# Kernel optimization log

Hardware: AMD Instinct MI355X
Metric: run time of the kernel (lower is better)

## Reference

```python
import jax, jax.numpy as jnp
import numpy as np

B, T, C = 2, 2048, 1024
NUM_HEADS, QK_LEN, V_LEN = 16, 64, 64


def setup_inputs() -> dict:
    key = jax.random.key(0)
    ks = jax.random.split(key, 11)
    s = 0.02
    return {
        "Q": jax.random.normal(ks[0], (B, T, C), jnp.float32),
        "K": jax.random.normal(ks[1], (B, T, C), jnp.float32),
        "V": jax.random.normal(ks[2], (B, T, C), jnp.float32),
        # Linear weights stored as (in, out); y = x @ W + b
        "Wq": jax.random.normal(ks[3], (C, NUM_HEADS * QK_LEN), jnp.float32) * s,
        "bq": jnp.zeros((NUM_HEADS * QK_LEN,), jnp.float32),
        "Wk": jax.random.normal(ks[4], (C, NUM_HEADS * QK_LEN), jnp.float32) * s,
        "bk": jnp.zeros((NUM_HEADS * QK_LEN,), jnp.float32),
        "Wv": jax.random.normal(ks[5], (C, NUM_HEADS * V_LEN), jnp.float32) * s,
        "bv": jnp.zeros((NUM_HEADS * V_LEN,), jnp.float32),
        "Wo": jax.random.normal(ks[6], (NUM_HEADS * V_LEN, C), jnp.float32) * s,
        "bo": jnp.zeros((C,), jnp.float32),
    }


def _split_heads(x, n_heads, d):
    b, t, _ = x.shape
    return x.reshape(b, t, n_heads, d).transpose(0, 2, 1, 3)  # (B,H,T,d)


def reference(Q, K, V, Wq, bq, Wk, bk, Wv, bv, Wo, bo):
    q = _split_heads(Q @ Wq + bq, NUM_HEADS, QK_LEN)   # (B,H,T,dk)
    k = _split_heads(K @ Wk + bk, NUM_HEADS, QK_LEN)   # (B,H,T,dk)
    v = _split_heads(V @ Wv + bv, NUM_HEADS, V_LEN)    # (B,H,T,dv)

    scale = 1.0 / jnp.sqrt(jnp.asarray(QK_LEN, q.dtype))
    scores = jnp.einsum("bhqd,bhkd->bhqk", q, k) * scale  # (B,H,T,T)
    attn = jax.nn.softmax(scores, axis=-1)
    out = jnp.einsum("bhqk,bhkd->bhqd", attn, v)           # (B,H,T,dv)

    out = out.transpose(0, 2, 1, 3).reshape(Q.shape[0], Q.shape[1], NUM_HEADS * V_LEN)
    return out @ Wo + bo
```

## Files before the change

### kernel.cpp

```cpp
#include <hip/hip_runtime.h>
#include <hip/hip_bf16.h>
#include <math.h>

constexpr int B = 2, T = 2048, C = 1024, H = 16, D = 64;
constexpr int M = B * T;
constexpr float SCALE_L2E = 0.125f * 1.4426950408889634f;

typedef __attribute__((ext_vector_type(8))) short s16x8;
typedef __attribute__((ext_vector_type(4))) short s16x4;
typedef __attribute__((ext_vector_type(4))) float fv4;

typedef unsigned short ushort_t;

static __device__ __forceinline__ ushort_t f2bf(float x) {
    union { float f; unsigned u; } c; c.f = x;
    unsigned u = c.u + 0x7FFFu + ((c.u >> 16) & 1u);
    return (ushort_t)(u >> 16);
}

static __device__ __forceinline__ int cvt_pk_bf16(float lo, float hi) {
    int r;
    asm("v_cvt_pk_bf16_f32 %0, %1, %2" : "=v"(r) : "v"(lo), "v"(hi));
    return r;
}

#define GLDS(gp, lp) __builtin_amdgcn_global_load_lds( \
    (const __attribute__((address_space(1))) void*)(gp), \
    (__attribute__((address_space(3))) void*)(lp), 16, 0, 0)

__global__ __launch_bounds__(256) void convert_qkv(
    const float* __restrict__ Q, const float* __restrict__ K,
    const float* __restrict__ V, ushort_t* __restrict__ dst)
{
    size_t e = ((size_t)blockIdx.x * 256 + threadIdx.x) * 8;
    const float* src;
    size_t base;
    if (e < (size_t)M * C)          { src = Q; base = 0; }
    else if (e < 2 * (size_t)M * C) { src = K; base = (size_t)M * C; }
    else                            { src = V; base = 2 * (size_t)M * C; }
    const float* p = src + (e - base);
    float4 a = *(const float4*)p;
    float4 b = *(const float4*)(p + 4);
    union { s16x8 v; int i[4]; } o;
    o.i[0] = cvt_pk_bf16(a.x, a.y);
    o.i[1] = cvt_pk_bf16(a.z, a.w);
    o.i[2] = cvt_pk_bf16(b.x, b.y);
    o.i[3] = cvt_pk_bf16(b.z, b.w);
    *(s16x8*)(dst + e) = o.v;
}

__global__ __launch_bounds__(256) void transpose_w(
    const float* __restrict__ W0, const float* __restrict__ W1,
    const float* __restrict__ W2, const float* __restrict__ W3,
    ushort_t* __restrict__ Wt)
{
    const int s = blockIdx.z;
    const float* W = (s == 0) ? W0 : (s == 1) ? W1 : (s == 2) ? W2 : W3;
    const int k0 = blockIdx.x * 64, n0 = blockIdx.y * 64;
    __shared__ ushort_t tile[64][72];
    const int tid = threadIdx.x;
#pragma unroll
    for (int it = 0; it < 4; it++) {
        int f = it * 256 + tid;
        int r = f >> 4, c4 = (f & 15) * 4;
        float4 x = *(const float4*)(W + (size_t)(k0 + r) * C + n0 + c4);
        *(int*)&tile[r][c4]     = cvt_pk_bf16(x.x, x.y);
        *(int*)&tile[r][c4 + 2] = cvt_pk_bf16(x.z, x.w);
    }
    __syncthreads();
#pragma unroll
    for (int it = 0; it < 4; it++) {
        int f = it * 256 + tid;
        int rr = f >> 4, c4 = (f & 15) * 4;
        union { s16x4 v; ushort_t u[4]; } u;
#pragma unroll
        for (int j = 0; j < 4; j++) u.u[j] = tile[c4 + j][rr];
        *(s16x4*)(Wt + (size_t)(s * 1024 + n0 + rr) * 1024 + k0 + c4) = u.v;
    }
}

__global__ __launch_bounds__(256) void transpose_v(
    const ushort_t* __restrict__ vw, ushort_t* __restrict__ vt)
{
    __shared__ ushort_t tile[64][72];
    const int tid = threadIdx.x;
    const int t0 = blockIdx.x * 64;
    const int bh = blockIdx.y;
    const ushort_t* src = vw + ((size_t)bh * T + t0) * D;
#pragma unroll
    for (int it = 0; it < 2; it++) {
        int f = it * 256 + tid;
        int row = f >> 3, c8 = (f & 7) * 8;
        *(s16x8*)&tile[row][c8] = *(const s16x8*)(src + (size_t)row * D + c8);
    }
    __syncthreads();
    ushort_t* dst = vt + (size_t)bh * D * T + t0;
#pragma unroll
    for (int it = 0; it < 4; it++) {
        int f = it * 256 + tid;
        int d = f >> 4, t4 = (f & 15) * 4;
        union { s16x4 v; ushort_t u[4]; } u;
#pragma unroll
        for (int j = 0; j < 4; j++) u.u[j] = tile[t4 + j][d];
        *(s16x4*)(dst + (size_t)d * T + t4) = u.v;
    }
}

__global__ __launch_bounds__(256) void gemm_qkv(
    const ushort_t* __restrict__ qkv, const ushort_t* __restrict__ Wt,
    const float* __restrict__ bq, const float* __restrict__ bk,
    const float* __restrict__ bv,
    ushort_t* __restrict__ qw, ushort_t* __restrict__ kw,
    ushort_t* __restrict__ vw)
{
    __shared__ ushort_t As[2][128 * 32];
    __shared__ ushort_t Bs[2][128 * 32];

    const int tid = threadIdx.x;
    const int w = tid >> 6, lane = tid & 63;
    const int quad = lane >> 4, lc = lane & 15;
    const int wm = w & 1, wn = w >> 1;

    const int nt = blockIdx.x;
    const int m0 = blockIdx.y * 128;
    const int s = nt >> 3;
    const int nsec0 = (nt & 7) * 128;

    const ushort_t* Abase = qkv + (size_t)s * M * C;
    const ushort_t* Btbase = Wt + (size_t)nt * 128 * 1024;

    const int srow = (w << 4) + (lane >> 2);
    const int ske  = (lane & 3) * 8;

    fv4 acc[4][4] = {};

    auto stage = [&](int k0, int buf) {
#pragma unroll
        for (int i = 0; i < 2; i++) {
            int row = i * 64 + srow;
            GLDS(Abase + (size_t)(m0 + row) * 1024 + k0 + ske,
                 As[buf] + i * 2048 + w * 512);
            GLDS(Btbase + (size_t)row * 1024 + k0 + ske,
                 Bs[buf] + i * 2048 + w * 512);
        }
    };

    stage(0, 0);
    __syncthreads();

    for (int k0 = 0; k0 < 1024; k0 += 32) {
        const int cur = (k0 >> 5) & 1;
        if (k0 + 32 < 1024) stage(k0 + 32, cur ^ 1);

        s16x8 af[4], bf[4];
#pragma unroll
        for (int ms = 0; ms < 4; ms++)
            af[ms] = *(const s16x8*)(As[cur] + (wm * 64 + ms * 16 + lc) * 32 + quad * 8);
#pragma unroll
        for (int ns = 0; ns < 4; ns++)
            bf[ns] = *(const s16x8*)(Bs[cur] + (wn * 64 + ns * 16 + lc) * 32 + quad * 8);
#pragma unroll
        for (int ms = 0; ms < 4; ms++)
#pragma unroll
            for (int ns = 0; ns < 4; ns++)
                acc[ms][ns] = __builtin_amdgcn_mfma_f32_16x16x32_bf16(
                    af[ms], bf[ns], acc[ms][ns], 0, 0, 0);
        __syncthreads();
    }

    const float* biasp = (s == 0) ? bq : (s == 1) ? bk : bv;
    const float premul = (s == 0) ? SCALE_L2E : 1.0f;
    ushort_t* outp = (s == 0) ? qw : (s == 1) ? kw : vw;

#pragma unroll
    for (int ns = 0; ns < 4; ns++) {
        const int nl = nsec0 + wn * 64 + ns * 16 + lc;
        const float bias = biasp[nl];
        const int h_ = nl >> 6, d_ = nl & 63;
#pragma unroll
        for (int ms = 0; ms < 4; ms++) {
#pragma unroll
            for (int r = 0; r < 4; r++) {
                int m = m0 + wm * 64 + ms * 16 + quad * 4 + r;
                float val = (acc[ms][ns][r] + bias) * premul;
                int b_ = m >> 11, t_ = m & (T - 1);
                size_t bh = (size_t)(b_ * H + h_);
                outp[((bh * T + t_) << 6) + d_] = f2bf(val);
            }
        }
    }
}

__global__ __launch_bounds__(256) void gemm_final(
    const ushort_t* __restrict__ A, const ushort_t* __restrict__ Wot,
    const float* __restrict__ bo, float* __restrict__ out)
{
    __shared__ ushort_t As[2][128 * 32];
    __shared__ ushort_t Bs[2][64 * 32];

    const int tid = threadIdx.x;
    const int w = tid >> 6, lane = tid & 63;
    const int quad = lane >> 4, lc = lane & 15;
    const int wm = w & 1, wn = w >> 1;

    const int n0 = blockIdx.x * 64;
    const int m0 = blockIdx.y * 128;

    const int srow = (w << 4) + (lane >> 2);
    const int ske  = (lane & 3) * 8;

    fv4 acc[4][2] = {};

    auto stage = [&](int k0, int buf) {
        GLDS(A + (size_t)(m0 + srow) * 1024 + k0 + ske,      As[buf] + w * 512);
        GLDS(A + (size_t)(m0 + 64 + srow) * 1024 + k0 + ske, As[buf] + 2048 + w * 512);
        GLDS(Wot + (size_t)(n0 + srow) * 1024 + k0 + ske,    Bs[buf] + w * 512);
    };

    stage(0, 0);
    __syncthreads();

    for (int k0 = 0; k0 < 1024; k0 += 32) {
        const int cur = (k0 >> 5) & 1;
        if (k0 + 32 < 1024) stage(k0 + 32, cur ^ 1);

        s16x8 af[4], bf[2];
#pragma unroll
        for (int ms = 0; ms < 4; ms++)
            af[ms] = *(const s16x8*)(As[cur] + (wm * 64 + ms * 16 + lc) * 32 + quad * 8);
#pragma unroll
        for (int ns = 0; ns < 2; ns++)
            bf[ns] = *(const s16x8*)(Bs[cur] + (wn * 32 + ns * 16 + lc) * 32 + quad * 8);
#pragma unroll
        for (int ms = 0; ms < 4; ms++)
#pragma unroll
            for (int ns = 0; ns < 2; ns++)
                acc[ms][ns] = __builtin_amdgcn_mfma_f32_16x16x32_bf16(
                    af[ms], bf[ns], acc[ms][ns], 0, 0, 0);
        __syncthreads();
    }

#pragma unroll
    for (int ns = 0; ns < 2; ns++) {
        const int n = n0 + wn * 32 + ns * 16 + lc;
        const float bias = bo[n];
#pragma unroll
        for (int ms = 0; ms < 4; ms++) {
#pragma unroll
            for (int r = 0; r < 4; r++) {
                int m = m0 + wm * 64 + ms * 16 + quad * 4 + r;
                out[(size_t)m * 1024 + n] = acc[ms][ns][r] + bias;
            }
        }
    }
}

__global__ __launch_bounds__(256, 4) void attn(
    const ushort_t* __restrict__ q, const ushort_t* __restrict__ k,
    const ushort_t* __restrict__ vT, ushort_t* __restrict__ o)
{
    __shared__ alignas(16) ushort_t ks[2][64 * 64];
    __shared__ alignas(16) ushort_t vs[2][64 * 64];

    const int tid = threadIdx.x;
    const int w = tid >> 6, lane = tid & 63;
    const int quad = lane >> 4, lc = lane & 15;
    const int cs = lc & 7;
    const int qsub = w & 1, ksub = w >> 1;

    const int id = blockIdx.y * 32 + blockIdx.x;
    const int qt = (id >> 3) & 31;
    const int bh = (id & 7) * 4 + (id >> 8);

    s16x8 aq[2][2];
    const ushort_t* qb = q + ((size_t)bh * T + qt * 64 + qsub * 32) * D;
#pragma unroll
    for (int j = 0; j < 2; j++)
#pragma unroll
        for (int h = 0; h < 2; h++)
            aq[j][h] = *(const s16x8*)(qb + (size_t)(j * 16 + lc) * D + h * 32 + quad * 8);

    fv4 accO[2][4] = {};
    float psum[2] = {0.f, 0.f};

    const ushort_t* kb0 = k + (size_t)bh * T * D;
    const ushort_t* vb0 = vT + (size_t)bh * D * T;

    const int sr8 = lane >> 3;
    const int sch = (lane & 7) ^ sr8;

    auto stage = [&](int kt, int buf) {
#pragma unroll
        for (int i = 0; i < 2; i++) {
            const int r = w * 16 + i * 8 + sr8;
            GLDS(kb0 + (size_t)(kt * 64 + r) * 64 + sch * 8,
                 ks[buf] + (w * 16 + i * 8) * 64);
            GLDS(vb0 + (size_t)r * T + kt * 64 + sch * 8,
                 vs[buf] + (w * 16 + i * 8) * 64);
        }
    };

    stage(0, 0);
    __syncthreads();

    for (int kt = 0; kt < T / 64; kt++) {
        const int cur = kt & 1;
        if (kt + 1 < T / 64) stage(kt + 1, cur ^ 1);

        fv4 accST[2][2] = {};
        __builtin_amdgcn_s_setprio(1);
#pragma unroll
        for (int t4k = 0; t4k < 2; t4k++) {
            const int row = ksub * 32 + t4k * 16 + lc;
            s16x8 ak0 = *(const s16x8*)(ks[cur] + row * 64 + ((quad ^ cs) << 3));
            s16x8 ak1 = *(const s16x8*)(ks[cur] + row * 64 + (((quad + 4) ^ cs) << 3));
#pragma unroll
            for (int j = 0; j < 2; j++) {
                accST[j][t4k] = __builtin_amdgcn_mfma_f32_16x16x32_bf16(
                    ak0, aq[j][0], accST[j][t4k], 0, 0, 0);
                accST[j][t4k] = __builtin_amdgcn_mfma_f32_16x16x32_bf16(
                    ak1, aq[j][1], accST[j][t4k], 0, 0, 0);
            }
        }
        __builtin_amdgcn_s_setprio(0);

        s16x8 av[4];
#pragma unroll
        for (int t4v = 0; t4v < 4; t4v++) {
            const int row = t4v * 16 + lc;
            av[t4v] = *(const s16x8*)(vs[cur] + row * 64 + (((ksub * 4 + quad) ^ cs) << 3));
        }

#pragma unroll
        for (int j = 0; j < 2; j++) {
            float p0 = __builtin_amdgcn_exp2f(accST[j][0][0]);
            float p1 = __builtin_amdgcn_exp2f(accST[j][0][1]);
            float p2 = __builtin_amdgcn_exp2f(accST[j][0][2]);
            float p3 = __builtin_amdgcn_exp2f(accST[j][0][3]);
            float p4 = __builtin_amdgcn_exp2f(accST[j][1][0]);
            float p5 = __builtin_amdgcn_exp2f(accST[j][1][1]);
            float p6 = __builtin_amdgcn_exp2f(accST[j][1][2]);
            float p7 = __builtin_amdgcn_exp2f(accST[j][1][3]);
            psum[j] += ((p0 + p1) + (p2 + p3)) + ((p4 + p5) + (p6 + p7));

            int W00 = cvt_pk_bf16(p0, p1);
            int W01 = cvt_pk_bf16(p2, p3);
            int W10 = cvt_pk_bf16(p4, p5);
            int W11 = cvt_pk_bf16(p6, p7);
            asm("v_permlane32_swap_b32 %0, %1" : "+v"(W00), "+v"(W10));
            asm("v_permlane16_swap_b32 %0, %1" : "+v"(W00), "+v"(W10));
            asm("v_permlane32_swap_b32 %0, %1" : "+v"(W01), "+v"(W11));
            asm("v_permlane16_swap_b32 %0, %1" : "+v"(W01), "+v"(W11));

            union { int i[4]; s16x8 v; } pbu;
            pbu.i[0] = W00; pbu.i[1] = W01; pbu.i[2] = W10; pbu.i[3] = W11;

            __builtin_amdgcn_s_setprio(1);
#pragma unroll
            for (int t4v = 0; t4v < 4; t4v++)
                accO[j][t4v] = __builtin_amdgcn_mfma_f32_16x16x32_bf16(
                    av[t4v], pbu.v, accO[j][t4v], 0, 0, 0);
            __builtin_amdgcn_s_setprio(0);
        }

        __syncthreads();
    }

#pragma unroll
    for (int j = 0; j < 2; j++) {
        psum[j] += __shfl_xor(psum[j], 16);
        psum[j] += __shfl_xor(psum[j], 32);
    }

    float* sc = (float*)&ks[0][0];
#pragma unroll
    for (int c = 0; c < 4; c++) {
        const int j = c >> 1, tv = (c & 1) * 2;
        __syncthreads();
        if (ksub == 1) {
            *(fv4*)(sc + ((qsub * 64 + lane) * 8))     = accO[j][tv];
            *(fv4*)(sc + ((qsub * 64 + lane) * 8 + 4)) = accO[j][tv + 1];
        }
        __syncthreads();
        if (ksub == 0) {
            accO[j][tv]     += *(fv4*)(sc + ((qsub * 64 + lane) * 8));
            accO[j][tv + 1] += *(fv4*)(sc + ((qsub * 64 + lane) * 8 + 4));
        }
    }
    __syncthreads();
    if (ksub == 1) {
        sc[(qsub * 64 + lane) * 2]     = psum[0];
        sc[(qsub * 64 + lane) * 2 + 1] = psum[1];
    }
    __syncthreads();
    if (ksub == 0) {
        psum[0] += sc[(qsub * 64 + lane) * 2];
        psum[1] += sc[(qsub * 64 + lane) * 2 + 1];

        const int b_ = bh >> 4, h_ = bh & 15;
#pragma unroll
        for (int j = 0; j < 2; j++) {
            float inv = 1.0f / psum[j];
            int row = qt * 64 + qsub * 32 + j * 16 + lc;
            ushort_t* op = o + ((size_t)b_ * T + row) * C + h_ * 64;
#pragma unroll
            for (int t4v = 0; t4v < 4; t4v++) {
                union { s16x4 v; int i[2]; } u;
                u.i[0] = cvt_pk_bf16(accO[j][t4v][0] * inv, accO[j][t4v][1] * inv);
                u.i[1] = cvt_pk_bf16(accO[j][t4v][2] * inv, accO[j][t4v][3] * inv);
                *(s16x4*)(op + t4v * 16 + quad * 4) = u.v;
            }
        }
    }
}

extern "C" void kernel_launch(void* const* d_in, const int* in_sizes, int n_in,
                              void* d_out, int out_size, void* d_ws, size_t ws_size,
                              hipStream_t stream)
{
    const float* Q  = (const float*)d_in[0];
    const float* K  = (const float*)d_in[1];
    const float* V  = (const float*)d_in[2];
    const float* Wq = (const float*)d_in[3];
    const float* bq = (const float*)d_in[4];
    const float* Wk = (const float*)d_in[5];
    const float* bk = (const float*)d_in[6];
    const float* Wv = (const float*)d_in[7];
    const float* bv = (const float*)d_in[8];
    const float* Wo = (const float*)d_in[9];
    const float* bo = (const float*)d_in[10];
    float* out = (float*)d_out;

    ushort_t* qkvbf = (ushort_t*)d_ws;
    ushort_t* Wt = qkvbf + (size_t)3 * M * C;
    ushort_t* qw = Wt + (size_t)4096 * 1024;
    ushort_t* kw = qw + (size_t)M * C;
    ushort_t* vw = kw + (size_t)M * C;
    ushort_t* vt = vw + (size_t)M * C;
    ushort_t* ow = qkvbf;
    ushort_t* Wot = Wt + (size_t)3072 * 1024;

    dim3 blk(256);
    convert_qkv<<<dim3(3 * M * C / 2048), blk, 0, stream>>>(Q, K, V, qkvbf);
    transpose_w<<<dim3(16, 16, 4), blk, 0, stream>>>(Wq, Wk, Wv, Wo, Wt);
    gemm_qkv<<<dim3(24, 32), blk, 0, stream>>>(qkvbf, Wt, bq, bk, bv, qw, kw, vw);
    transpose_v<<<dim3(T / 64, B * H), blk, 0, stream>>>(vw, vt);
    attn<<<dim3(T / 64, B * H), blk, 0, stream>>>(qw, kw, vt, ow);
    gemm_final<<<dim3(16, 32), blk, 0, stream>>>(ow, Wot, bo, out);
}
```

Before: 235.7 us.

## Give each wave a private key slice and drop per-tile block barriers

Attention work is redistributed so each of the four waves processes all 64 queries against its own 16-key slice of every 64-key tile. Each wave stages its K and V^T slice into its own LDS region and waits with s_waitcnt on its own loads, so the per-iteration __syncthreads is gone. The catch is that the P·V MFMA is fed half-zero operands, which doubles P·V MFMA issue. Register use also rises (accO[4][4]), so launch bounds drop to 3 blocks, and the end-of-kernel cross-wave reduction of four partial outputs through LDS is larger.

```diff
diff --git a/kernel.cpp b/kernel.cpp
--- a/kernel.cpp
+++ b/kernel.cpp
@@ -255,98 +255,78 @@
     }
 }
 
-__global__ __launch_bounds__(256, 4) void attn(
+__global__ __launch_bounds__(256, 3) void attn(
     const ushort_t* __restrict__ q, const ushort_t* __restrict__ k,
     const ushort_t* __restrict__ vT, ushort_t* __restrict__ o)
 {
-    __shared__ alignas(16) ushort_t ks[2][64 * 64];
-    __shared__ alignas(16) ushort_t vs[2][64 * 64];
+    __shared__ alignas(16) ushort_t ks[2][4][1024];
+    __shared__ alignas(16) ushort_t vs[2][4][1024];
 
     const int tid = threadIdx.x;
     const int w = tid >> 6, lane = tid & 63;
     const int quad = lane >> 4, lc = lane & 15;
     const int cs = lc & 7;
-    const int qsub = w & 1, ksub = w >> 1;
 
     const int id = blockIdx.y * 32 + blockIdx.x;
     const int qt = (id >> 3) & 31;
     const int bh = (id & 7) * 4 + (id >> 8);
 
-    s16x8 aq[2][2];
-    const ushort_t* qb = q + ((size_t)bh * T + qt * 64 + qsub * 32) * D;
-#pragma unroll
-    for (int j = 0; j < 2; j++)
+    s16x8 aq[4][2];
+    const ushort_t* qb = q + ((size_t)bh * T + qt * 64) * D;
+#pragma unroll
+    for (int j = 0; j < 4; j++)
 #pragma unroll
         for (int h = 0; h < 2; h++)
             aq[j][h] = *(const s16x8*)(qb + (size_t)(j * 16 + lc) * D + h * 32 + quad * 8);
 
-    fv4 accO[2][4] = {};
-    float psum[2] = {0.f, 0.f};
-
-    const ushort_t* kb0 = k + (size_t)bh * T * D;
-    const ushort_t* vb0 = vT + (size_t)bh * D * T;
-
-    const int sr8 = lane >> 3;
-    const int sch = (lane & 7) ^ sr8;
+    fv4 accO[4][4] = {};
+    float psum[4] = {0.f, 0.f, 0.f, 0.f};
+
+    const ushort_t* kb0 = k + (size_t)bh * T * D
+        + (size_t)(w * 16 + (lane >> 3)) * 64 + (((lane & 7) ^ ((lane >> 3) & 7)) * 8);
+    const ushort_t* vb0 = vT + (size_t)bh * D * T
+        + (size_t)(lane >> 1) * T + w * 16 + (lane & 1) * 8;
 
     auto stage = [&](int kt, int buf) {
-#pragma unroll
-        for (int i = 0; i < 2; i++) {
-            const int r = w * 16 + i * 8 + sr8;
-            GLDS(kb0 + (size_t)(kt * 64 + r) * 64 + sch * 8,
-                 ks[buf] + (w * 16 + i * 8) * 64);
-            GLDS(vb0 + (size_t)r * T + kt * 64 + sch * 8,
-                 vs[buf] + (w * 16 + i * 8) * 64);
-        }
+        GLDS(kb0 + (size_t)kt * 4096,          &ks[buf][w][0]);
+        GLDS(kb0 + (size_t)kt * 4096 + 512,    &ks[buf][w][512]);
+        GLDS(vb0 + kt * 64,                    &vs[buf][w][0]);
+        GLDS(vb0 + kt * 64 + (size_t)32 * T,   &vs[buf][w][512]);
     };
 
-    stage(0, 0);
-    __syncthreads();
-
-    for (int kt = 0; kt < T / 64; kt++) {
-        const int cur = kt & 1;
-        if (kt + 1 < T / 64) stage(kt + 1, cur ^ 1);
-
-        fv4 accST[2][2] = {};
+    auto body = [&](int cur) {
+        const ushort_t* ksw = &ks[cur][w][0];
+        const ushort_t* vsw = &vs[cur][w][0];
+
+        s16x8 ak0 = *(const s16x8*)(ksw + lc * 64 + ((quad ^ cs) << 3));
+        s16x8 ak1 = *(const s16x8*)(ksw + lc * 64 + (((quad + 4) ^ cs) << 3));
+
+        fv4 accST[4];
         __builtin_amdgcn_s_setprio(1);
 #pragma unroll
-        for (int t4k = 0; t4k < 2; t4k++) {
-            const int row = ksub * 32 + t4k * 16 + lc;
-            s16x8 ak0 = *(const s16x8*)(ks[cur] + row * 64 + ((quad ^ cs) << 3));
-            s16x8 ak1 = *(const s16x8*)(ks[cur] + row * 64 + (((quad + 4) ^ cs) << 3));
-#pragma unroll
-            for (int j = 0; j < 2; j++) {
-                accST[j][t4k] = __builtin_amdgcn_mfma_f32_16x16x32_bf16(
-                    ak0, aq[j][0], accST[j][t4k], 0, 0, 0);
-                accST[j][t4k] = __builtin_amdgcn_mfma_f32_16x16x32_bf16(
-                    ak1, aq[j][1], accST[j][t4k], 0, 0, 0);
-            }
+        for (int j = 0; j < 4; j++) {
+            fv4 z = {};
+            z = __builtin_amdgcn_mfma_f32_16x16x32_bf16(ak0, aq[j][0], z, 0, 0, 0);
+            accST[j] = __builtin_amdgcn_mfma_f32_16x16x32_bf16(ak1, aq[j][1], z, 0, 0, 0);
         }
         __builtin_amdgcn_s_setprio(0);
 
         s16x8 av[4];
 #pragma unroll
-        for (int t4v = 0; t4v < 4; t4v++) {
-            const int row = t4v * 16 + lc;
-            av[t4v] = *(const s16x8*)(vs[cur] + row * 64 + (((ksub * 4 + quad) ^ cs) << 3));
-        }
-
-#pragma unroll
-        for (int j = 0; j < 2; j++) {
-            float p0 = __builtin_amdgcn_exp2f(accST[j][0][0]);
-            float p1 = __builtin_amdgcn_exp2f(accST[j][0][1]);
-            float p2 = __builtin_amdgcn_exp2f(accST[j][0][2]);
-            float p3 = __builtin_amdgcn_exp2f(accST[j][0][3]);
-            float p4 = __builtin_amdgcn_exp2f(accST[j][1][0]);
-            float p5 = __builtin_amdgcn_exp2f(accST[j][1][1]);
-            float p6 = __builtin_amdgcn_exp2f(accST[j][1][2]);
-            float p7 = __builtin_amdgcn_exp2f(accST[j][1][3]);
-            psum[j] += ((p0 + p1) + (p2 + p3)) + ((p4 + p5) + (p6 + p7));
+        for (int t4v = 0; t4v < 4; t4v++)
+            av[t4v] = *(const s16x8*)(vsw + (t4v * 16 + lc) * 16 + ((quad & 1) << 3));
+
+#pragma unroll
+        for (int j = 0; j < 4; j++) {
+            float p0 = __builtin_amdgcn_exp2f(accST[j][0]);
+            float p1 = __builtin_amdgcn_exp2f(accST[j][1]);
+            float p2 = __builtin_amdgcn_exp2f(accST[j][2]);
+            float p3 = __builtin_amdgcn_exp2f(accST[j][3]);
+            psum[j] += (p0 + p1) + (p2 + p3);
 
             int W00 = cvt_pk_bf16(p0, p1);
             int W01 = cvt_pk_bf16(p2, p3);
-            int W10 = cvt_pk_bf16(p4, p5);
-            int W11 = cvt_pk_bf16(p6, p7);
+            int W10 = 0, W11 = 0;
             asm("v_permlane32_swap_b32 %0, %1" : "+v"(W00), "+v"(W10));
             asm("v_permlane16_swap_b32 %0, %1" : "+v"(W00), "+v"(W10));
             asm("v_permlane32_swap_b32 %0, %1" : "+v"(W01), "+v"(W11));
@@ -362,46 +342,74 @@
                     av[t4v], pbu.v, accO[j][t4v], 0, 0, 0);
             __builtin_amdgcn_s_setprio(0);
         }
-
-        __syncthreads();
-    }
-
-#pragma unroll
-    for (int j = 0; j < 2; j++) {
+    };
+
+    stage(0, 0);
+    for (int kt = 0; kt < T / 64 - 1; kt++) {
+        stage(kt + 1, (kt & 1) ^ 1);
+        asm volatile("s_waitcnt vmcnt(4)" ::: "memory");
+        body(kt & 1);
+    }
+    asm volatile("s_waitcnt vmcnt(0)" ::: "memory");
+    body(1);
+
+#pragma unroll
+    for (int j = 0; j < 4; j++) {
         psum[j] += __shfl_xor(psum[j], 16);
         psum[j] += __shfl_xor(psum[j], 32);
     }
 
-    float* sc = (float*)&ks[0][0];
-#pragma unroll
-    for (int c = 0; c < 4; c++) {
-        const int j = c >> 1, tv = (c & 1) * 2;
-        __syncthreads();
-        if (ksub == 1) {
-            *(fv4*)(sc + ((qsub * 64 + lane) * 8))     = accO[j][tv];
-            *(fv4*)(sc + ((qsub * 64 + lane) * 8 + 4)) = accO[j][tv + 1];
-        }
-        __syncthreads();
-        if (ksub == 0) {
-            accO[j][tv]     += *(fv4*)(sc + ((qsub * 64 + lane) * 8));
-            accO[j][tv + 1] += *(fv4*)(sc + ((qsub * 64 + lane) * 8 + 4));
-        }
-    }
-    __syncthreads();
-    if (ksub == 1) {
-        sc[(qsub * 64 + lane) * 2]     = psum[0];
-        sc[(qsub * 64 + lane) * 2 + 1] = psum[1];
-    }
-    __syncthreads();
-    if (ksub == 0) {
-        psum[0] += sc[(qsub * 64 + lane) * 2];
-        psum[1] += sc[(qsub * 64 + lane) * 2 + 1];
+    float* scA = (float*)&ks[0][0][0];
+    float* scB = (float*)&vs[0][0][0];
+
+    __syncthreads();
+    if (w) { fv4 t = {psum[0], psum[1], psum[2], psum[3]};
+             *(fv4*)(scA + (w - 1) * 256 + lane * 4) = t; }
+    __syncthreads();
+    if (w == 0) {
+#pragma unroll
+        for (int ww = 0; ww < 3; ww++) {
+            fv4 t = *(const fv4*)(scA + ww * 256 + lane * 4);
+#pragma unroll
+            for (int j = 0; j < 4; j++) psum[j] += t[j];
+        }
+    }
+    __syncthreads();
+
+    if (w == 2)
+#pragma unroll
+        for (int c = 0; c < 16; c++)
+            *(fv4*)(scA + lane * 64 + c * 4) = accO[c >> 2][c & 3];
+    if (w == 3)
+#pragma unroll
+        for (int c = 0; c < 16; c++)
+            *(fv4*)(scB + lane * 64 + c * 4) = accO[c >> 2][c & 3];
+    __syncthreads();
+    if (w == 0)
+#pragma unroll
+        for (int c = 0; c < 16; c++)
+            accO[c >> 2][c & 3] += *(const fv4*)(scA + lane * 64 + c * 4);
+    if (w == 1)
+#pragma unroll
+        for (int c = 0; c < 16; c++)
+            accO[c >> 2][c & 3] += *(const fv4*)(scB + lane * 64 + c * 4);
+    __syncthreads();
+    if (w == 1)
+#pragma unroll
+        for (int c = 0; c < 16; c++)
+            *(fv4*)(scA + lane * 64 + c * 4) = accO[c >> 2][c & 3];
+    __syncthreads();
+
+    if (w == 0) {
+#pragma unroll
+        for (int c = 0; c < 16; c++)
+            accO[c >> 2][c & 3] += *(const fv4*)(scA + lane * 64 + c * 4);
 
         const int b_ = bh >> 4, h_ = bh & 15;
 #pragma unroll
-        for (int j = 0; j < 2; j++) {
+        for (int j = 0; j < 4; j++) {
             float inv = 1.0f / psum[j];
-            int row = qt * 64 + qsub * 32 + j * 16 + lc;
+            int row = qt * 64 + j * 16 + lc;
             ushort_t* op = o + ((size_t)b_ * T + row) * C + h_ * 64;
 #pragma unroll
             for (int t4v = 0; t4v < 4; t4v++) {
```

After: 258.0 us. 1.09x slower.

## Merge input conversion with weight transpose and write V transposed from QKV GEMM

Applied to the files above, without the earlier changes.

Merges the fp32-to-bf16 conversion of Q/K/V and the weight transpose into a single launch, indexed by block range. The QKV projection epilogue now writes V directly in the d-major transposed layout the attention kernel wants, which removes the separate transpose_v kernel and its extra read/write pass. This drops two launches and one intermediate buffer. The cost is that V stores become strided writes of 4 contiguous bf16 values, which may coalesce less well than before.

```diff
diff --git a/kernel.cpp b/kernel.cpp
--- a/kernel.cpp
+++ b/kernel.cpp
@@ -28,37 +28,39 @@
     (const __attribute__((address_space(1))) void*)(gp), \
     (__attribute__((address_space(3))) void*)(lp), 16, 0, 0)
 
-__global__ __launch_bounds__(256) void convert_qkv(
+__global__ __launch_bounds__(256) void prep(
     const float* __restrict__ Q, const float* __restrict__ K,
-    const float* __restrict__ V, ushort_t* __restrict__ dst)
-{
-    size_t e = ((size_t)blockIdx.x * 256 + threadIdx.x) * 8;
-    const float* src;
-    size_t base;
-    if (e < (size_t)M * C)          { src = Q; base = 0; }
-    else if (e < 2 * (size_t)M * C) { src = K; base = (size_t)M * C; }
-    else                            { src = V; base = 2 * (size_t)M * C; }
-    const float* p = src + (e - base);
-    float4 a = *(const float4*)p;
-    float4 b = *(const float4*)(p + 4);
-    union { s16x8 v; int i[4]; } o;
-    o.i[0] = cvt_pk_bf16(a.x, a.y);
-    o.i[1] = cvt_pk_bf16(a.z, a.w);
-    o.i[2] = cvt_pk_bf16(b.x, b.y);
-    o.i[3] = cvt_pk_bf16(b.z, b.w);
-    *(s16x8*)(dst + e) = o.v;
-}
-
-__global__ __launch_bounds__(256) void transpose_w(
+    const float* __restrict__ V,
     const float* __restrict__ W0, const float* __restrict__ W1,
     const float* __restrict__ W2, const float* __restrict__ W3,
-    ushort_t* __restrict__ Wt)
+    ushort_t* __restrict__ dst, ushort_t* __restrict__ Wt)
 {
-    const int s = blockIdx.z;
-    const float* W = (s == 0) ? W0 : (s == 1) ? W1 : (s == 2) ? W2 : W3;
-    const int k0 = blockIdx.x * 64, n0 = blockIdx.y * 64;
     __shared__ ushort_t tile[64][72];
     const int tid = threadIdx.x;
+
+    if (blockIdx.x < 6144) {
+        size_t e = ((size_t)blockIdx.x * 256 + tid) * 8;
+        const float* src;
+        size_t base;
+        if (e < (size_t)M * C)          { src = Q; base = 0; }
+        else if (e < 2 * (size_t)M * C) { src = K; base = (size_t)M * C; }
+        else                            { src = V; base = 2 * (size_t)M * C; }
+        const float* p = src + (e - base);
+        float4 a = *(const float4*)p;
+        float4 b = *(const float4*)(p + 4);
+        union { s16x8 v; int i[4]; } o;
+        o.i[0] = cvt_pk_bf16(a.x, a.y);
+        o.i[1] = cvt_pk_bf16(a.z, a.w);
+        o.i[2] = cvt_pk_bf16(b.x, b.y);
+        o.i[3] = cvt_pk_bf16(b.z, b.w);
+        *(s16x8*)(dst + e) = o.v;
+        return;
+    }
+
+    const int idx = blockIdx.x - 6144;
+    const int s = idx >> 8;
+    const float* W = (s == 0) ? W0 : (s == 1) ? W1 : (s == 2) ? W2 : W3;
+    const int k0 = (idx & 15) * 64, n0 = ((idx >> 4) & 15) * 64;
 #pragma unroll
     for (int it = 0; it < 4; it++) {
         int f = it * 256 + tid;
@@ -79,39 +81,12 @@
     }
 }
 
-__global__ __launch_bounds__(256) void transpose_v(
-    const ushort_t* __restrict__ vw, ushort_t* __restrict__ vt)
-{
-    __shared__ ushort_t tile[64][72];
-    const int tid = threadIdx.x;
-    const int t0 = blockIdx.x * 64;
-    const int bh = blockIdx.y;
-    const ushort_t* src = vw + ((size_t)bh * T + t0) * D;
-#pragma unroll
-    for (int it = 0; it < 2; it++) {
-        int f = it * 256 + tid;
-        int row = f >> 3, c8 = (f & 7) * 8;
-        *(s16x8*)&tile[row][c8] = *(const s16x8*)(src + (size_t)row * D + c8);
-    }
-    __syncthreads();
-    ushort_t* dst = vt + (size_t)bh * D * T + t0;
-#pragma unroll
-    for (int it = 0; it < 4; it++) {
-        int f = it * 256 + tid;
-        int d = f >> 4, t4 = (f & 15) * 4;
-        union { s16x4 v; ushort_t u[4]; } u;
-#pragma unroll
-        for (int j = 0; j < 4; j++) u.u[j] = tile[t4 + j][d];
-        *(s16x4*)(dst + (size_t)d * T + t4) = u.v;
-    }
-}
-
 __global__ __launch_bounds__(256) void gemm_qkv(
     const ushort_t* __restrict__ qkv, const ushort_t* __restrict__ Wt,
     const float* __restrict__ bq, const float* __restrict__ bk,
     const float* __restrict__ bv,
     ushort_t* __restrict__ qw, ushort_t* __restrict__ kw,
-    ushort_t* __restrict__ vw)
+    ushort_t* __restrict__ vt)
 {
     __shared__ ushort_t As[2][128 * 32];
     __shared__ ushort_t Bs[2][128 * 32];
@@ -168,9 +143,29 @@
         __syncthreads();
     }
 
-    const float* biasp = (s == 0) ? bq : (s == 1) ? bk : bv;
+    if (s == 2) {
+#pragma unroll
+        for (int ns = 0; ns < 4; ns++) {
+            const int nl = nsec0 + wn * 64 + ns * 16 + lc;
+            const float bias = bv[nl];
+            const int h_ = nl >> 6, d_ = nl & 63;
+#pragma unroll
+            for (int ms = 0; ms < 4; ms++) {
+                int m = m0 + wm * 64 + ms * 16 + quad * 4;
+                int b_ = m >> 11, t_ = m & (T - 1);
+                size_t row = (size_t)(b_ * H + h_) * 64 + d_;
+                union { s16x4 v; int i[2]; } u;
+                u.i[0] = cvt_pk_bf16(acc[ms][ns][0] + bias, acc[ms][ns][1] + bias);
+                u.i[1] = cvt_pk_bf16(acc[ms][ns][2] + bias, acc[ms][ns][3] + bias);
+                *(s16x4*)(vt + row * T + t_) = u.v;
+            }
+        }
+        return;
+    }
+
+    const float* biasp = (s == 0) ? bq : bk;
     const float premul = (s == 0) ? SCALE_L2E : 1.0f;
-    ushort_t* outp = (s == 0) ? qw : (s == 1) ? kw : vw;
+    ushort_t* outp = (s == 0) ? qw : kw;
 
 #pragma unroll
     for (int ns = 0; ns < 4; ns++) {
@@ -435,16 +430,13 @@
     ushort_t* Wt = qkvbf + (size_t)3 * M * C;
     ushort_t* qw = Wt + (size_t)4096 * 1024;
     ushort_t* kw = qw + (size_t)M * C;
-    ushort_t* vw = kw + (size_t)M * C;
-    ushort_t* vt = vw + (size_t)M * C;
+    ushort_t* vt = kw + (size_t)M * C;
     ushort_t* ow = qkvbf;
     ushort_t* Wot = Wt + (size_t)3072 * 1024;
 
     dim3 blk(256);
-    convert_qkv<<<dim3(3 * M * C / 2048), blk, 0, stream>>>(Q, K, V, qkvbf);
-    transpose_w<<<dim3(16, 16, 4), blk, 0, stream>>>(Wq, Wk, Wv, Wo, Wt);
-    gemm_qkv<<<dim3(24, 32), blk, 0, stream>>>(qkvbf, Wt, bq, bk, bv, qw, kw, vw);
-    transpose_v<<<dim3(T / 64, B * H), blk, 0, stream>>>(vw, vt);
+    prep<<<dim3(7168), blk, 0, stream>>>(Q, K, V, Wq, Wk, Wv, Wo, qkvbf, Wt);
+    gemm_qkv<<<dim3(24, 32), blk, 0, stream>>>(qkvbf, Wt, bq, bk, bv, qw, kw, vt);
     attn<<<dim3(T / 64, B * H), blk, 0, stream>>>(qw, kw, vt, ow);
     gemm_final<<<dim3(16, 32), blk, 0, stream>>>(ow, Wot, bo, out);
 }
```

Result: slower. 248.8 us (+5.6%).
